# Kernel tuning notes

Measured on AMD Instinct MI355X. Metric: run time of the kernel, lower is better.

## Reference

```python
import jax, jax.numpy as jnp
import numpy as np

WS = 8      # window size
SS = 4      # shift size
NH = 4      # num heads
EPS = 1e-5
MLP_RATIO = 4


def _win_part(x, ws):
    # x: [B,D,H,W,C] -> [B*nD*nH*nW, ws^3, C]
    B, D, H, W, C = x.shape
    x = x.reshape(B, D // ws, ws, H // ws, ws, W // ws, ws, C)
    x = x.transpose(0, 1, 3, 5, 2, 4, 6, 7)
    return x.reshape(-1, ws * ws * ws, C)


def _win_rev(w, ws, B, D, H, W):
    C = w.shape[-1]
    x = w.reshape(B, D // ws, H // ws, W // ws, ws, ws, ws, C)
    x = x.transpose(0, 1, 4, 2, 5, 3, 6, 7)
    return x.reshape(B, D, H, W, C)


def _ln(x, g, b):
    m = jnp.mean(x, axis=-1, keepdims=True)
    v = jnp.mean((x - m) ** 2, axis=-1, keepdims=True)
    return (x - m) / jnp.sqrt(v + EPS) * g + b


def _rel_index(ws):
    coords = np.stack(np.meshgrid(np.arange(ws), np.arange(ws), np.arange(ws), indexing='ij'))  # [3,ws,ws,ws]
    cf = coords.reshape(3, -1)                      # [3, ws^3]
    rel = (cf[:, :, None] - cf[:, None, :]).transpose(1, 2, 0) + (ws - 1)  # [N,N,3]
    return rel[..., 0] * (2 * ws - 1) ** 2 + rel[..., 1] * (2 * ws - 1) + rel[..., 2]


def _attn_mask(D, H, W, ws, ss):
    img = np.zeros((1, D, H, W, 1), dtype=np.float32)
    cnt = 0
    sl = (slice(0, -ws), slice(-ws, -ss), slice(-ss, None))
    for d in sl:
        for h in sl:
            for w in sl:
                img[:, d, h, w, :] = cnt
                cnt += 1
    mw = np.asarray(_win_part(jnp.asarray(img), ws))[..., 0]  # [nW, ws^3]
    diff = mw[:, None, :] - mw[:, :, None]
    return np.where(diff != 0, -100.0, 0.0).astype(np.float32)


def setup_inputs() -> dict:
    key = jax.random.key(0)
    ks = jax.random.split(key, 12)
    B, D, H, W, C = 1, 16, 64, 64, 128
    mh = MLP_RATIO * C
    s = 0.02
    return {
        'x': jax.random.normal(ks[0], (B, D, H, W, C), jnp.float32),
        'attn_mask': jnp.asarray(_attn_mask(D, H, W, WS, SS)),
        'rel_index': jnp.asarray(_rel_index(WS), jnp.int32),
        'rel_bias': jax.random.normal(ks[1], ((2 * WS - 1) ** 3, NH), jnp.float32) * s,
        'qkv_w': jax.random.normal(ks[2], (3 * C, C), jnp.float32) * s,
        'qkv_b': jnp.zeros((3 * C,), jnp.float32),
        'proj_w': jax.random.normal(ks[3], (C, C), jnp.float32) * s,
        'proj_b': jnp.zeros((C,), jnp.float32),
        'norm1_g': jnp.ones((C,), jnp.float32),
        'norm1_b': jnp.zeros((C,), jnp.float32),
        'norm2_g': jnp.ones((C,), jnp.float32),
        'norm2_b': jnp.zeros((C,), jnp.float32),
        'mlp_w1': jax.random.normal(ks[4], (mh, C), jnp.float32) * s,
        'mlp_b1': jnp.zeros((mh,), jnp.float32),
        'mlp_w2': jax.random.normal(ks[5], (C, mh), jnp.float32) * s,
        'mlp_b2': jnp.zeros((C,), jnp.float32),
    }


def reference(x, attn_mask, rel_index, rel_bias, qkv_w, qkv_b, proj_w, proj_b,
              norm1_g, norm1_b, norm2_g, norm2_b, mlp_w1, mlp_b1, mlp_w2, mlp_b2):
    B, D, H, W, C = x.shape
    ws, ss, nh = WS, SS, NH
    hd = C // nh
    scale = hd ** -0.5
    N = ws ** 3
    shortcut = x
    h = _ln(x, norm1_g, norm1_b)
    h = jnp.roll(h, (-ss, -ss, -ss), axis=(1, 2, 3))
    xw = _win_part(h, ws)                 # [B_, N, C]
    B_ = xw.shape[0]
    nW = attn_mask.shape[0]
    qkv = xw @ qkv_w.T + qkv_b            # [B_, N, 3C]
    qkv = qkv.reshape(B_, N, 3, nh, hd).transpose(2, 0, 3, 1, 4)  # [3,B_,h,N,hd]
    q, k, v = qkv[0] * scale, qkv[1], qkv[2]
    attn = jnp.einsum('bhnd,bhmd->bhnm', q, k)
    rpe = rel_bias[rel_index.reshape(-1)].reshape(N, N, nh).transpose(2, 0, 1)  # [h,N,N]
    attn = attn + rpe[None]
    attn = attn.reshape(B_ // nW, nW, nh, N, N) + attn_mask[None, :, None]
    attn = jax.nn.softmax(attn.reshape(B_, nh, N, N), axis=-1)
    out = jnp.einsum('bhnm,bhmd->bhnd', attn, v).transpose(0, 2, 1, 3).reshape(B_, N, C)
    out = out @ proj_w.T + proj_b
    out = _win_rev(out, ws, B, D, H, W)
    out = jnp.roll(out, (ss, ss, ss), axis=(1, 2, 3))
    x = shortcut + out
    h2 = _ln(x, norm2_g, norm2_b)
    h2 = jax.nn.gelu(h2 @ mlp_w1.T + mlp_b1, approximate=False)
    return x + h2 @ mlp_w2.T + mlp_b2
```

## Files before the change

### kernel.cpp

```cpp
#include <hip/hip_runtime.h>
#include <math.h>

typedef __bf16 bf16;
typedef __bf16 bf16x4 __attribute__((ext_vector_type(4)));
typedef __bf16 bf16x8 __attribute__((ext_vector_type(8)));
typedef float f32x4 __attribute__((ext_vector_type(4)));
typedef unsigned short u16;
typedef u16 u16x2 __attribute__((ext_vector_type(2)));

#define LOG2E 1.4426950408889634f

__device__ __forceinline__ float b2f(u16 b) {
  return (float)__builtin_bit_cast(bf16, b);
}

__global__ void sniff_k(const unsigned* __restrict__ xw_, int* __restrict__ flag) {
  int lane = threadIdx.x;
  int c = 0;
#pragma unroll
  for (int j = 0; j < 4; j++) {
    unsigned e = (xw_[lane * 4 + j] >> 7) & 0xFFu;
    c += (e >= 100u && e <= 140u) ? 1 : 0;
  }
#pragma unroll
  for (int d = 1; d < 64; d <<= 1) c += __shfl_xor(c, d);
  if (lane == 0) *flag = (c >= 150) ? 1 : 0;
}

__global__ __launch_bounds__(256) void canon_big_k(const void* __restrict__ src,
                                                   bf16* __restrict__ dst,
                                                   const int* __restrict__ flag) {
  int i = (blockIdx.x * 256 + threadIdx.x) * 8;
  if (*flag) {
    *(bf16x8*)&dst[i] = *(const bf16x8*)((const bf16*)src + i);
  } else {
    const float* s = (const float*)src + i;
    bf16x8 v;
#pragma unroll
    for (int j = 0; j < 8; j++) v[j] = (bf16)s[j];
    *(bf16x8*)&dst[i] = v;
  }
}

struct CanonArgs {
  const void* src[13];
  bf16* dst[13];
  int n[13];
};

__global__ __launch_bounds__(256) void canon_small_k(CanonArgs a,
                                                     const int* __restrict__ flag) {
  int ti = blockIdx.y;
  int i = blockIdx.x * 256 + threadIdx.x;
  if (i >= a.n[ti]) return;
  if (*flag)
    a.dst[ti][i] = ((const bf16*)a.src[ti])[i];
  else
    a.dst[ti][i] = (bf16)((const float*)a.src[ti])[i];
}

__global__ __launch_bounds__(256) void rpe_k(const int* __restrict__ ridx,
                                             const bf16* __restrict__ rbias,
                                             bf16* __restrict__ rpe) {
  int t = blockIdx.x * 256 + threadIdx.x;
  int m = t & 511, q = (t >> 9) & 511, h = t >> 18;
  rpe[t] = (bf16)((float)rbias[ridx[q * 512 + m] * 4 + h] * LOG2E);
}

template <int ROLL>
__global__ __launch_bounds__(256) void ln_k(const bf16* __restrict__ x,
                                            const bf16* __restrict__ g,
                                            const bf16* __restrict__ bsh,
                                            bf16* __restrict__ out) {
  int wave = threadIdx.x >> 6, lane = threadIdx.x & 63;
  int tok = blockIdx.x * 4 + wave;
  size_t src;
  if (ROLL) {
    int win = tok >> 9, pos = tok & 511;
    int rd = (win >> 6) * 8 + (pos >> 6);
    int rh = ((win >> 3) & 7) * 8 + ((pos >> 3) & 7);
    int rw = (win & 7) * 8 + (pos & 7);
    int od = (rd + 4) & 15, oh = (rh + 4) & 63, ow = (rw + 4) & 63;
    src = (size_t)((od * 64 + oh) * 64 + ow) * 128;
  } else {
    src = (size_t)tok * 128;
  }
  int ch = lane * 2;
  u16x2 xv = *(const u16x2*)(x + src + ch);
  float f0 = b2f(xv[0]), f1 = b2f(xv[1]);
  float s = f0 + f1, sq = f0 * f0 + f1 * f1;
#pragma unroll
  for (int d = 1; d < 64; d <<= 1) {
    s += __shfl_xor(s, d);
    sq += __shfl_xor(sq, d);
  }
  float mean = s * (1.f / 128.f);
  float var = sq * (1.f / 128.f) - mean * mean;
  float rstd = rsqrtf(fmaxf(var, 0.f) + 1e-5f);
  u16x2 gv = *(const u16x2*)(g + ch), bv = *(const u16x2*)(bsh + ch);
  u16x2 ov;
  ov[0] = __builtin_bit_cast(u16, (bf16)((f0 - mean) * rstd * b2f(gv[0]) + b2f(bv[0])));
  ov[1] = __builtin_bit_cast(u16, (bf16)((f1 - mean) * rstd * b2f(gv[1]) + b2f(bv[1])));
  *(u16x2*)(out + (size_t)tok * 128 + ch) = ov;
}

template <int EPI, int N_, int K_>
__global__ __launch_bounds__(256) void gemm_k(const bf16* __restrict__ A,
                                              const bf16* __restrict__ B,
                                              const bf16* __restrict__ bias,
                                              void* __restrict__ outv,
                                              const bf16* __restrict__ resid,
                                              const int* __restrict__ flag) {
  __shared__ __align__(16) u16 As[128 * 72];
  __shared__ __align__(16) u16 Bs[128 * 72];
  const int t = threadIdx.x;
  const int wave = t >> 6, lane = t & 63, l15 = lane & 15, quad = lane >> 4;
  const int m0 = blockIdx.x * 128, n0 = blockIdx.y * 128;
  int fl = 0;
  if constexpr (EPI == 3) fl = *flag;
  f32x4 acc[4][4] = {};
  const int wr = (wave >> 1) * 64, wc = (wave & 1) * 64;
  const int srow = t >> 3, scol = (t & 7) * 8;
  constexpr int NC = K_ / 64;
  bf16x8 avA[4], avB[4];
#pragma unroll
  for (int p = 0; p < 4; p++) {
    int row = p * 32 + srow;
    avA[p] = *(const bf16x8*)(A + (size_t)(m0 + row) * K_ + scol);
  }
#pragma unroll
  for (int c = 0; c < NC; c++) {
    const bf16x8* av = (c & 1) ? avB : avA;
    bf16x8* avN = (c & 1) ? avA : avB;
    if (c + 1 < NC) {
#pragma unroll
      for (int p = 0; p < 4; p++) {
        int row = p * 32 + srow;
        avN[p] = *(const bf16x8*)(A + (size_t)(m0 + row) * K_ + (c + 1) * 64 + scol);
      }
    }
    bf16x8 bv[4];
#pragma unroll
    for (int p = 0; p < 4; p++) {
      int row = p * 32 + srow;
      bv[p] = *(const bf16x8*)(B + (size_t)(n0 + row) * K_ + c * 64 + scol);
    }
    __syncthreads();
#pragma unroll
    for (int p = 0; p < 4; p++) {
      int row = p * 32 + srow;
      *(bf16x8*)&As[row * 72 + scol] = av[p];
      *(bf16x8*)&Bs[row * 72 + scol] = bv[p];
    }
    __syncthreads();
#pragma unroll
    for (int ks = 0; ks < 2; ks++) {
      bf16x8 a[4], b[4];
#pragma unroll
      for (int i = 0; i < 4; i++) {
        a[i] = *(const bf16x8*)&As[(wr + i * 16 + l15) * 72 + ks * 32 + quad * 8];
        b[i] = *(const bf16x8*)&Bs[(wc + i * 16 + l15) * 72 + ks * 32 + quad * 8];
      }
#pragma unroll
      for (int i = 0; i < 4; i++)
#pragma unroll
        for (int j = 0; j < 4; j++)
          acc[i][j] =
              __builtin_amdgcn_mfma_f32_16x16x32_bf16(a[i], b[j], acc[i][j], 0, 0, 0);
    }
  }
  const float qscale = 0.17677669529663687f * LOG2E;
#pragma unroll
  for (int i = 0; i < 4; i++) {
#pragma unroll
    for (int r = 0; r < 4; r++) {
      int tok = m0 + wr + i * 16 + quad * 4 + r;
      size_t obase = 0;
      if constexpr (EPI == 1) {
        int win = tok >> 9, pos = tok & 511;
        int rd = (win >> 6) * 8 + (pos >> 6);
        int rh = ((win >> 3) & 7) * 8 + ((pos >> 3) & 7);
        int rw = (win & 7) * 8 + (pos & 7);
        int od = (rd + 4) & 15, oh = (rh + 4) & 63, ow = (rw + 4) & 63;
        obase = (size_t)((od * 64 + oh) * 64 + ow) * 128;
      } else if constexpr (EPI != 0) {
        obase = (size_t)tok * N_;
      }
#pragma unroll
      for (int j = 0; j < 4; j++) {
        int gn = n0 + wc + j * 16 + l15;
        float v = acc[i][j][r] + (float)bias[gn];
        if constexpr (EPI == 0) {
          int tensor = gn >> 7, c = gn & 127, head = c >> 5, d = c & 31;
          if (tensor == 0) v *= qscale;
          int win = tok >> 9, pos = tok & 511;
          size_t off = ((((size_t)tensor * 4 + head) * 128 + win) * 512 + pos) * 32 + d;
          ((bf16*)outv)[off] = (bf16)v;
        } else if constexpr (EPI == 1) {
          v += (float)resid[obase + gn];
          ((bf16*)outv)[obase + gn] = (bf16)v;
        } else if constexpr (EPI == 2) {
          float v2 = v * v;
          float u2 = v * (2.30220806f + 0.10294323f * v2);
          float e2 = exp2f(u2);
          float rcp = __builtin_amdgcn_rcpf(e2 + 1.f);
          v = v - v * rcp;
          ((bf16*)outv)[obase + gn] = (bf16)v;
        } else {
          v += (float)resid[obase + gn];
          if (fl)
            ((bf16*)outv)[obase + gn] = (bf16)v;
          else
            ((float*)outv)[obase + gn] = v;
        }
      }
    }
  }
}

__global__ __launch_bounds__(256) void attn_k(const bf16* __restrict__ qkv,
                                              const bf16* __restrict__ rpe,
                                              bf16* __restrict__ att) {
  __shared__ __align__(16) bf16 sVt[32 * 264];
  __shared__ __align__(16) bf16 sP[4][32 * 72];
  __shared__ __align__(4) unsigned char lbl[512];
  const int t = threadIdx.x;
  const int p = blockIdx.x;
  const int win = ((p >> 7) << 3) | (p & 7);
  const int j = (p >> 3) & 15;
  const int head = j >> 2, qc = j & 3;
  const int wave = t >> 6, lane = t & 63, l15 = lane & 15, quad = lane >> 4;

  const int wd = win >> 6, wh = (win >> 3) & 7, ww = win & 7;
  const bool wm = (wd == 1) || (wh == 7) || (ww == 7);
  if (wm) {
    for (int pp = t; pp < 512; pp += 256) {
      int gd = wd * 8 + (pp >> 6), gh = wh * 8 + ((pp >> 3) & 7),
          gw = ww * 8 + (pp & 7);
      int ld = gd < 8 ? 0 : (gd < 12 ? 1 : 2);
      int lh = gh < 56 ? 0 : (gh < 60 ? 1 : 2);
      int lw = gw < 56 ? 0 : (gw < 60 ? 1 : 2);
      lbl[pp] = (unsigned char)((ld << 4) | (lh << 2) | lw);
    }
  }

  const size_t hw32 = (size_t)512 * 32;
  const bf16* qp = qkv + ((size_t)(0 * 4 + head) * 128 + win) * hw32;
  const bf16* kp = qkv + ((size_t)(1 * 4 + head) * 128 + win) * hw32;
  const bf16* vp = qkv + ((size_t)(2 * 4 + head) * 128 + win) * hw32;
  const bf16* rpeh = rpe + (size_t)head * 512 * 512;
  const int qbase = qc * 128 + wave * 32;

  bf16x8 qa[2];
#pragma unroll
  for (int nt = 0; nt < 2; nt++)
    qa[nt] = *(const bf16x8*)(qp + (size_t)(qbase + nt * 16 + l15) * 32 + quad * 8);

  f32x4 O[2][2] = {};
  float ms[2] = {-1e30f, -1e30f}, ls[2] = {0.f, 0.f};
  int lq[2] = {0, 0};
  bf16* pw = sP[wave];

  for (int half = 0; half < 2; half++) {
    if (half) __syncthreads();
    {
      int kpi = t >> 3, dblk = (t & 7) * 4;
      unsigned* s32 = (unsigned*)sVt;
#pragma unroll
      for (int kb = 0; kb < 4; kb++) {
        const bf16* v0 = vp + (size_t)(half * 256 + kb * 64 + 2 * kpi) * 32 + dblk;
        bf16x4 a = *(const bf16x4*)v0;
        bf16x4 b = *(const bf16x4*)(v0 + 32);
        int keyw = kb * 32 + kpi;
#pragma unroll
        for (int dd = 0; dd < 4; dd++) {
          unsigned wv = (unsigned)__builtin_bit_cast(u16, a[dd]) |
                        ((unsigned)__builtin_bit_cast(u16, b[dd]) << 16);
          s32[(dblk + dd) * 132 + keyw] = wv;
        }
      }
    }
    __syncthreads();
    if (half == 0 && wm) {
#pragma unroll
      for (int nt = 0; nt < 2; nt++) lq[nt] = lbl[qbase + nt * 16 + l15];
    }

#pragma unroll 2
    for (int kt4 = 0; kt4 < 4; kt4++) {
      const int kt = half * 4 + kt4;
      f32x4 S[4][2];
#pragma unroll
      for (int mt = 0; mt < 4; mt++) {
        bf16x8 kb =
            *(const bf16x8*)(kp + (size_t)(kt * 64 + mt * 16 + l15) * 32 + quad * 8);
        int kcb = kt * 64 + mt * 16 + quad * 4;
        unsigned kl4 = 0;
        if (wm) kl4 = *(const unsigned*)&lbl[kcb];
#pragma unroll
        for (int nt = 0; nt < 2; nt++) {
          bf16x4 rv =
              *(const bf16x4*)(rpeh + (size_t)(qbase + nt * 16 + l15) * 512 + kcb);
          f32x4 c;
#pragma unroll
          for (int r = 0; r < 4; r++) {
            float bv = (float)rv[r];
            if (wm && (int)((kl4 >> (8 * r)) & 0xFF) != lq[nt]) bv -= 144.269504f;
            c[r] = bv;
          }
          S[mt][nt] = __builtin_amdgcn_mfma_f32_16x16x32_bf16(kb, qa[nt], c, 0, 0, 0);
        }
      }
#pragma unroll
      for (int nt = 0; nt < 2; nt++) {
        float mx = -1e30f;
#pragma unroll
        for (int mt = 0; mt < 4; mt++)
#pragma unroll
          for (int r = 0; r < 4; r++) mx = fmaxf(mx, S[mt][nt][r]);
        mx = fmaxf(mx, __shfl_xor(mx, 16));
        mx = fmaxf(mx, __shfl_xor(mx, 32));
        float mnew = fmaxf(ms[nt], mx);
        float alpha = exp2f(ms[nt] - mnew);
        ms[nt] = mnew;
        float rs = 0.f;
#pragma unroll
        for (int mt = 0; mt < 4; mt++)
#pragma unroll
          for (int r = 0; r < 4; r++) {
            float pe = exp2f(S[mt][nt][r] - mnew);
            S[mt][nt][r] = pe;
            rs += pe;
          }
        rs += __shfl_xor(rs, 16);
        rs += __shfl_xor(rs, 32);
        ls[nt] = ls[nt] * alpha + rs;
        O[0][nt] *= alpha;
        O[1][nt] *= alpha;
      }
#pragma unroll
      for (int nt = 0; nt < 2; nt++)
#pragma unroll
        for (int mt = 0; mt < 4; mt++) {
          bf16x4 pv;
#pragma unroll
          for (int r = 0; r < 4; r++) pv[r] = (bf16)S[mt][nt][r];
          *(bf16x4*)&pw[(nt * 16 + l15) * 72 + mt * 16 + quad * 4] = pv;
        }
#pragma unroll
      for (int s = 0; s < 2; s++) {
        bf16x8 va0 =
            *(const bf16x8*)&sVt[l15 * 264 + kt4 * 64 + s * 32 + quad * 8];
        bf16x8 va1 =
            *(const bf16x8*)&sVt[(16 + l15) * 264 + kt4 * 64 + s * 32 + quad * 8];
        bf16x8 pb0 = *(const bf16x8*)&pw[l15 * 72 + s * 32 + quad * 8];
        bf16x8 pb1 = *(const bf16x8*)&pw[(16 + l15) * 72 + s * 32 + quad * 8];
        O[0][0] = __builtin_amdgcn_mfma_f32_16x16x32_bf16(va0, pb0, O[0][0], 0, 0, 0);
        O[0][1] = __builtin_amdgcn_mfma_f32_16x16x32_bf16(va0, pb1, O[0][1], 0, 0, 0);
        O[1][0] = __builtin_amdgcn_mfma_f32_16x16x32_bf16(va1, pb0, O[1][0], 0, 0, 0);
        O[1][1] = __builtin_amdgcn_mfma_f32_16x16x32_bf16(va1, pb1, O[1][1], 0, 0, 0);
      }
    }
  }
#pragma unroll
  for (int nt = 0; nt < 2; nt++) {
    float inv = __builtin_amdgcn_rcpf(ls[nt]);
    int q = qbase + nt * 16 + l15;
#pragma unroll
    for (int dm = 0; dm < 2; dm++) {
      bf16x4 o;
#pragma unroll
      for (int r = 0; r < 4; r++) o[r] = (bf16)(O[dm][nt][r] * inv);
      *(bf16x4*)(att + ((size_t)win * 512 + q) * 128 + head * 32 + dm * 16 +
                 quad * 4) = o;
    }
  }
}

extern "C" void kernel_launch(void* const* d_in, const int* in_sizes, int n_in,
                              void* d_out, int out_size, void* d_ws,
                              size_t ws_size, hipStream_t stream) {
  const int* rel_index = (const int*)d_in[2];
  char* w = (char*)d_ws;

  int* flag = (int*)w;
  bf16* rb_c = (bf16*)(w + (64ull << 10));
  bf16* qw_c = (bf16*)(w + (128ull << 10));
  bf16* pw_c = (bf16*)(w + (256ull << 10));
  bf16* w1_c = (bf16*)(w + (320ull << 10));
  bf16* w2_c = (bf16*)(w + (512ull << 10));
  bf16* qb_c = (bf16*)(w + (704ull << 10));
  bf16* pb_c = (bf16*)(w + (708ull << 10));
  bf16* g1_c = (bf16*)(w + (712ull << 10));
  bf16* b1n_c = (bf16*)(w + (716ull << 10));
  bf16* g2_c = (bf16*)(w + (720ull << 10));
  bf16* b2n_c = (bf16*)(w + (724ull << 10));
  bf16* mb1_c = (bf16*)(w + (728ull << 10));
  bf16* mb2_c = (bf16*)(w + (732ull << 10));
  bf16* x_c = (bf16*)(w + (1ull << 20));
  bf16* xw = (bf16*)(w + (17ull << 20));
  bf16* qkvb = (bf16*)(w + (33ull << 20));
  bf16* rpe = (bf16*)(w + (97ull << 20));
  bf16* x2 = (bf16*)(w + (99ull << 20));
  bf16* att = xw;
  bf16* h2 = xw;
  bf16* a1 = qkvb;

  sniff_k<<<1, 64, 0, stream>>>((const unsigned*)d_in[0], flag);
  canon_big_k<<<4096, 256, 0, stream>>>(d_in[0], x_c, flag);

  CanonArgs ca;
  const int srcidx[13] = {3, 4, 5, 6, 7, 8, 9, 10, 11, 12, 13, 14, 15};
  bf16* dsts[13] = {rb_c, qw_c, qb_c, pw_c, pb_c, g1_c, b1n_c,
                    g2_c, b2n_c, w1_c, mb1_c, w2_c, mb2_c};
  for (int i = 0; i < 13; i++) {
    ca.src[i] = d_in[srcidx[i]];
    ca.dst[i] = dsts[i];
    ca.n[i] = in_sizes[srcidx[i]];
  }
  canon_small_k<<<dim3(256, 13), 256, 0, stream>>>(ca, flag);

  rpe_k<<<4096, 256, 0, stream>>>(rel_index, rb_c, rpe);
  ln_k<1><<<16384, 256, 0, stream>>>(x_c, g1_c, b1n_c, xw);
  gemm_k<0, 384, 128><<<dim3(512, 3), 256, 0, stream>>>(xw, qw_c, qb_c, qkvb,
                                                        nullptr, flag);
  attn_k<<<2048, 256, 0, stream>>>(qkvb, rpe, att);
  gemm_k<1, 128, 128><<<dim3(512, 1), 256, 0, stream>>>(att, pw_c, pb_c, x2,
                                                        x_c, flag);
  ln_k<0><<<16384, 256, 0, stream>>>(x2, g2_c, b2n_c, h2);
  gemm_k<2, 512, 128><<<dim3(512, 4), 256, 0, stream>>>(h2, w1_c, mb1_c, a1,
                                                        nullptr, flag);
  gemm_k<3, 128, 512><<<dim3(512, 1), 256, 0, stream>>>(a1, w2_c, mb2_c, d_out,
                                                        x2, flag);
}
```

Baseline: 449.5 us.

## Halve GEMM M-tile for narrow GEMMs and stage full V window once in attention

The GEMM kernel takes its M tile size as a template parameter, and the two N=128 GEMMs (proj and MLP down) now use 64-row tiles on 1024 blocks so more blocks are resident across CUs. The attention kernel now transposes all 512 keys of V into shared memory once up front, instead of in two halves with a block barrier between them, and runs a single 8-step key loop. This removes a mid-loop barrier and the reload phase, but roughly doubles attention LDS use, which may cut occupancy.

```diff
diff --git a/kernel.cpp b/kernel.cpp
--- a/kernel.cpp
+++ b/kernel.cpp
@@ -104,27 +104,29 @@
   *(u16x2*)(out + (size_t)tok * 128 + ch) = ov;
 }
 
-template <int EPI, int N_, int K_>
+template <int EPI, int BM, int N_, int K_>
 __global__ __launch_bounds__(256) void gemm_k(const bf16* __restrict__ A,
                                               const bf16* __restrict__ B,
                                               const bf16* __restrict__ bias,
                                               void* __restrict__ outv,
                                               const bf16* __restrict__ resid,
                                               const int* __restrict__ flag) {
-  __shared__ __align__(16) u16 As[128 * 72];
+  __shared__ __align__(16) u16 As[BM * 72];
   __shared__ __align__(16) u16 Bs[128 * 72];
   const int t = threadIdx.x;
   const int wave = t >> 6, lane = t & 63, l15 = lane & 15, quad = lane >> 4;
-  const int m0 = blockIdx.x * 128, n0 = blockIdx.y * 128;
+  const int m0 = blockIdx.x * BM, n0 = blockIdx.y * 128;
+  constexpr int MI = BM / 32;
+  constexpr int PA = BM / 32;
   int fl = 0;
   if constexpr (EPI == 3) fl = *flag;
-  f32x4 acc[4][4] = {};
-  const int wr = (wave >> 1) * 64, wc = (wave & 1) * 64;
+  f32x4 acc[MI][4] = {};
+  const int wr = (wave >> 1) * (BM / 2), wc = (wave & 1) * 64;
   const int srow = t >> 3, scol = (t & 7) * 8;
   constexpr int NC = K_ / 64;
-  bf16x8 avA[4], avB[4];
-#pragma unroll
-  for (int p = 0; p < 4; p++) {
+  bf16x8 avA[PA], avB[PA];
+#pragma unroll
+  for (int p = 0; p < PA; p++) {
     int row = p * 32 + srow;
     avA[p] = *(const bf16x8*)(A + (size_t)(m0 + row) * K_ + scol);
   }
@@ -134,7 +136,7 @@
     bf16x8* avN = (c & 1) ? avA : avB;
     if (c + 1 < NC) {
 #pragma unroll
-      for (int p = 0; p < 4; p++) {
+      for (int p = 0; p < PA; p++) {
         int row = p * 32 + srow;
         avN[p] = *(const bf16x8*)(A + (size_t)(m0 + row) * K_ + (c + 1) * 64 + scol);
       }
@@ -147,22 +149,23 @@
     }
     __syncthreads();
 #pragma unroll
-    for (int p = 0; p < 4; p++) {
-      int row = p * 32 + srow;
-      *(bf16x8*)&As[row * 72 + scol] = av[p];
-      *(bf16x8*)&Bs[row * 72 + scol] = bv[p];
-    }
+    for (int p = 0; p < PA; p++)
+      *(bf16x8*)&As[(p * 32 + srow) * 72 + scol] = av[p];
+#pragma unroll
+    for (int p = 0; p < 4; p++)
+      *(bf16x8*)&Bs[(p * 32 + srow) * 72 + scol] = bv[p];
     __syncthreads();
 #pragma unroll
     for (int ks = 0; ks < 2; ks++) {
-      bf16x8 a[4], b[4];
-#pragma unroll
-      for (int i = 0; i < 4; i++) {
+      bf16x8 a[MI], b[4];
+#pragma unroll
+      for (int i = 0; i < MI; i++)
         a[i] = *(const bf16x8*)&As[(wr + i * 16 + l15) * 72 + ks * 32 + quad * 8];
-        b[i] = *(const bf16x8*)&Bs[(wc + i * 16 + l15) * 72 + ks * 32 + quad * 8];
-      }
-#pragma unroll
-      for (int i = 0; i < 4; i++)
+#pragma unroll
+      for (int j = 0; j < 4; j++)
+        b[j] = *(const bf16x8*)&Bs[(wc + j * 16 + l15) * 72 + ks * 32 + quad * 8];
+#pragma unroll
+      for (int i = 0; i < MI; i++)
 #pragma unroll
         for (int j = 0; j < 4; j++)
           acc[i][j] =
@@ -171,7 +174,7 @@
   }
   const float qscale = 0.17677669529663687f * LOG2E;
 #pragma unroll
-  for (int i = 0; i < 4; i++) {
+  for (int i = 0; i < MI; i++) {
 #pragma unroll
     for (int r = 0; r < 4; r++) {
       int tok = m0 + wr + i * 16 + quad * 4 + r;
@@ -221,7 +224,7 @@
 __global__ __launch_bounds__(256) void attn_k(const bf16* __restrict__ qkv,
                                               const bf16* __restrict__ rpe,
                                               bf16* __restrict__ att) {
-  __shared__ __align__(16) bf16 sVt[32 * 264];
+  __shared__ __align__(16) bf16 sVt[32 * 520];
   __shared__ __align__(16) bf16 sP[4][32 * 72];
   __shared__ __align__(4) unsigned char lbl[512];
   const int t = threadIdx.x;
@@ -251,115 +254,111 @@
   const bf16* rpeh = rpe + (size_t)head * 512 * 512;
   const int qbase = qc * 128 + wave * 32;
 
+  {
+    int kpi = t >> 3, dblk = (t & 7) * 4;
+    unsigned* s32 = (unsigned*)sVt;
+#pragma unroll
+    for (int kb = 0; kb < 8; kb++) {
+      const bf16* v0 = vp + (size_t)(kb * 64 + 2 * kpi) * 32 + dblk;
+      bf16x4 a = *(const bf16x4*)v0;
+      bf16x4 b = *(const bf16x4*)(v0 + 32);
+      int keyw = (kb * 64 + 2 * kpi) >> 1;
+#pragma unroll
+      for (int dd = 0; dd < 4; dd++) {
+        unsigned wv = (unsigned)__builtin_bit_cast(u16, a[dd]) |
+                      ((unsigned)__builtin_bit_cast(u16, b[dd]) << 16);
+        s32[(dblk + dd) * 260 + keyw] = wv;
+      }
+    }
+  }
+
   bf16x8 qa[2];
 #pragma unroll
   for (int nt = 0; nt < 2; nt++)
     qa[nt] = *(const bf16x8*)(qp + (size_t)(qbase + nt * 16 + l15) * 32 + quad * 8);
 
+  __syncthreads();
+
+  int lq[2] = {0, 0};
+  if (wm) {
+#pragma unroll
+    for (int nt = 0; nt < 2; nt++) lq[nt] = lbl[qbase + nt * 16 + l15];
+  }
+
   f32x4 O[2][2] = {};
   float ms[2] = {-1e30f, -1e30f}, ls[2] = {0.f, 0.f};
-  int lq[2] = {0, 0};
   bf16* pw = sP[wave];
 
-  for (int half = 0; half < 2; half++) {
-    if (half) __syncthreads();
-    {
-      int kpi = t >> 3, dblk = (t & 7) * 4;
-      unsigned* s32 = (unsigned*)sVt;
-#pragma unroll
-      for (int kb = 0; kb < 4; kb++) {
-        const bf16* v0 = vp + (size_t)(half * 256 + kb * 64 + 2 * kpi) * 32 + dblk;
-        bf16x4 a = *(const bf16x4*)v0;
-        bf16x4 b = *(const bf16x4*)(v0 + 32);
-        int keyw = kb * 32 + kpi;
-#pragma unroll
-        for (int dd = 0; dd < 4; dd++) {
-          unsigned wv = (unsigned)__builtin_bit_cast(u16, a[dd]) |
-                        ((unsigned)__builtin_bit_cast(u16, b[dd]) << 16);
-          s32[(dblk + dd) * 132 + keyw] = wv;
+  for (int kt = 0; kt < 8; kt++) {
+    f32x4 S[4][2];
+#pragma unroll
+    for (int mt = 0; mt < 4; mt++) {
+      bf16x8 kb =
+          *(const bf16x8*)(kp + (size_t)(kt * 64 + mt * 16 + l15) * 32 + quad * 8);
+      int kcb = kt * 64 + mt * 16 + quad * 4;
+      unsigned kl4 = 0;
+      if (wm) kl4 = *(const unsigned*)&lbl[kcb];
+#pragma unroll
+      for (int nt = 0; nt < 2; nt++) {
+        bf16x4 rv =
+            *(const bf16x4*)(rpeh + (size_t)(qbase + nt * 16 + l15) * 512 + kcb);
+        f32x4 c;
+#pragma unroll
+        for (int r = 0; r < 4; r++) {
+          float bv = (float)rv[r];
+          if (wm && (int)((kl4 >> (8 * r)) & 0xFF) != lq[nt]) bv -= 144.269504f;
+          c[r] = bv;
         }
-      }
-    }
-    __syncthreads();
-    if (half == 0 && wm) {
-#pragma unroll
-      for (int nt = 0; nt < 2; nt++) lq[nt] = lbl[qbase + nt * 16 + l15];
-    }
-
-#pragma unroll 2
-    for (int kt4 = 0; kt4 < 4; kt4++) {
-      const int kt = half * 4 + kt4;
-      f32x4 S[4][2];
+        S[mt][nt] = __builtin_amdgcn_mfma_f32_16x16x32_bf16(kb, qa[nt], c, 0, 0, 0);
+      }
+    }
+#pragma unroll
+    for (int nt = 0; nt < 2; nt++) {
+      float mx = -1e30f;
+#pragma unroll
+      for (int mt = 0; mt < 4; mt++)
+#pragma unroll
+        for (int r = 0; r < 4; r++) mx = fmaxf(mx, S[mt][nt][r]);
+      mx = fmaxf(mx, __shfl_xor(mx, 16));
+      mx = fmaxf(mx, __shfl_xor(mx, 32));
+      float mnew = fmaxf(ms[nt], mx);
+      float alpha = exp2f(ms[nt] - mnew);
+      ms[nt] = mnew;
+      float rs = 0.f;
+#pragma unroll
+      for (int mt = 0; mt < 4; mt++)
+#pragma unroll
+        for (int r = 0; r < 4; r++) {
+          float pe = exp2f(S[mt][nt][r] - mnew);
+          S[mt][nt][r] = pe;
+          rs += pe;
+        }
+      rs += __shfl_xor(rs, 16);
+      rs += __shfl_xor(rs, 32);
+      ls[nt] = ls[nt] * alpha + rs;
+      O[0][nt] *= alpha;
+      O[1][nt] *= alpha;
+    }
+#pragma unroll
+    for (int nt = 0; nt < 2; nt++)
 #pragma unroll
       for (int mt = 0; mt < 4; mt++) {
-        bf16x8 kb =
-            *(const bf16x8*)(kp + (size_t)(kt * 64 + mt * 16 + l15) * 32 + quad * 8);
-        int kcb = kt * 64 + mt * 16 + quad * 4;
-        unsigned kl4 = 0;
-        if (wm) kl4 = *(const unsigned*)&lbl[kcb];
-#pragma unroll
-        for (int nt = 0; nt < 2; nt++) {
-          bf16x4 rv =
-              *(const bf16x4*)(rpeh + (size_t)(qbase + nt * 16 + l15) * 512 + kcb);
-          f32x4 c;
-#pragma unroll
-          for (int r = 0; r < 4; r++) {
-            float bv = (float)rv[r];
-            if (wm && (int)((kl4 >> (8 * r)) & 0xFF) != lq[nt]) bv -= 144.269504f;
-            c[r] = bv;
-          }
-          S[mt][nt] = __builtin_amdgcn_mfma_f32_16x16x32_bf16(kb, qa[nt], c, 0, 0, 0);
-        }
-      }
-#pragma unroll
-      for (int nt = 0; nt < 2; nt++) {
-        float mx = -1e30f;
-#pragma unroll
-        for (int mt = 0; mt < 4; mt++)
-#pragma unroll
-          for (int r = 0; r < 4; r++) mx = fmaxf(mx, S[mt][nt][r]);
-        mx = fmaxf(mx, __shfl_xor(mx, 16));
-        mx = fmaxf(mx, __shfl_xor(mx, 32));
-        float mnew = fmaxf(ms[nt], mx);
-        float alpha = exp2f(ms[nt] - mnew);
-        ms[nt] = mnew;
-        float rs = 0.f;
-#pragma unroll
-        for (int mt = 0; mt < 4; mt++)
-#pragma unroll
-          for (int r = 0; r < 4; r++) {
-            float pe = exp2f(S[mt][nt][r] - mnew);
-            S[mt][nt][r] = pe;
-            rs += pe;
-          }
-        rs += __shfl_xor(rs, 16);
-        rs += __shfl_xor(rs, 32);
-        ls[nt] = ls[nt] * alpha + rs;
-        O[0][nt] *= alpha;
-        O[1][nt] *= alpha;
-      }
-#pragma unroll
-      for (int nt = 0; nt < 2; nt++)
-#pragma unroll
-        for (int mt = 0; mt < 4; mt++) {
-          bf16x4 pv;
-#pragma unroll
-          for (int r = 0; r < 4; r++) pv[r] = (bf16)S[mt][nt][r];
-          *(bf16x4*)&pw[(nt * 16 + l15) * 72 + mt * 16 + quad * 4] = pv;
-        }
-#pragma unroll
-      for (int s = 0; s < 2; s++) {
-        bf16x8 va0 =
-            *(const bf16x8*)&sVt[l15 * 264 + kt4 * 64 + s * 32 + quad * 8];
-        bf16x8 va1 =
-            *(const bf16x8*)&sVt[(16 + l15) * 264 + kt4 * 64 + s * 32 + quad * 8];
-        bf16x8 pb0 = *(const bf16x8*)&pw[l15 * 72 + s * 32 + quad * 8];
-        bf16x8 pb1 = *(const bf16x8*)&pw[(16 + l15) * 72 + s * 32 + quad * 8];
-        O[0][0] = __builtin_amdgcn_mfma_f32_16x16x32_bf16(va0, pb0, O[0][0], 0, 0, 0);
-        O[0][1] = __builtin_amdgcn_mfma_f32_16x16x32_bf16(va0, pb1, O[0][1], 0, 0, 0);
-        O[1][0] = __builtin_amdgcn_mfma_f32_16x16x32_bf16(va1, pb0, O[1][0], 0, 0, 0);
-        O[1][1] = __builtin_amdgcn_mfma_f32_16x16x32_bf16(va1, pb1, O[1][1], 0, 0, 0);
-      }
+        bf16x4 pv;
+#pragma unroll
+        for (int r = 0; r < 4; r++) pv[r] = (bf16)S[mt][nt][r];
+        *(bf16x4*)&pw[(nt * 16 + l15) * 72 + mt * 16 + quad * 4] = pv;
+      }
+#pragma unroll
+    for (int s = 0; s < 2; s++) {
+      bf16x8 va0 = *(const bf16x8*)&sVt[l15 * 520 + kt * 64 + s * 32 + quad * 8];
+      bf16x8 va1 =
+          *(const bf16x8*)&sVt[(16 + l15) * 520 + kt * 64 + s * 32 + quad * 8];
+      bf16x8 pb0 = *(const bf16x8*)&pw[l15 * 72 + s * 32 + quad * 8];
+      bf16x8 pb1 = *(const bf16x8*)&pw[(16 + l15) * 72 + s * 32 + quad * 8];
+      O[0][0] = __builtin_amdgcn_mfma_f32_16x16x32_bf16(va0, pb0, O[0][0], 0, 0, 0);
+      O[0][1] = __builtin_amdgcn_mfma_f32_16x16x32_bf16(va0, pb1, O[0][1], 0, 0, 0);
+      O[1][0] = __builtin_amdgcn_mfma_f32_16x16x32_bf16(va1, pb0, O[1][0], 0, 0, 0);
+      O[1][1] = __builtin_amdgcn_mfma_f32_16x16x32_bf16(va1, pb1, O[1][1], 0, 0, 0);
     }
   }
 #pragma unroll
@@ -422,14 +421,14 @@
 
   rpe_k<<<4096, 256, 0, stream>>>(rel_index, rb_c, rpe);
   ln_k<1><<<16384, 256, 0, stream>>>(x_c, g1_c, b1n_c, xw);
-  gemm_k<0, 384, 128><<<dim3(512, 3), 256, 0, stream>>>(xw, qw_c, qb_c, qkvb,
-                                                        nullptr, flag);
+  gemm_k<0, 128, 384, 128><<<dim3(512, 3), 256, 0, stream>>>(xw, qw_c, qb_c,
+                                                             qkvb, nullptr, flag);
   attn_k<<<2048, 256, 0, stream>>>(qkvb, rpe, att);
-  gemm_k<1, 128, 128><<<dim3(512, 1), 256, 0, stream>>>(att, pw_c, pb_c, x2,
-                                                        x_c, flag);
+  gemm_k<1, 64, 128, 128><<<dim3(1024, 1), 256, 0, stream>>>(att, pw_c, pb_c,
+                                                             x2, x_c, flag);
   ln_k<0><<<16384, 256, 0, stream>>>(x2, g2_c, b2n_c, h2);
-  gemm_k<2, 512, 128><<<dim3(512, 4), 256, 0, stream>>>(h2, w1_c, mb1_c, a1,
-                                                        nullptr, flag);
-  gemm_k<3, 128, 512><<<dim3(512, 1), 256, 0, stream>>>(a1, w2_c, mb2_c, d_out,
-                                                        x2, flag);
-}
+  gemm_k<2, 128, 512, 128><<<dim3(512, 4), 256, 0, stream>>>(h2, w1_c, mb1_c,
+                                                             a1, nullptr, flag);
+  gemm_k<3, 64, 128, 512><<<dim3(1024, 1), 256, 0, stream>>>(a1, w2_c, mb2_c,
+                                                             d_out, x2, flag);
+}
```

Result: faster. 426.1 us (-5.2%).
